# Kernel optimization log

Hardware: AMD Instinct MI355X
Metric: run time of the kernel (lower is better)

Reference implementation:

```python
import jax, jax.numpy as jnp
import numpy as np

P = 12           # AR order == number of rollout steps
N = 2048         # input_size (nodes)
B = 128          # batch
C = 1            # channels (only channel 0 used)


def setup_inputs() -> dict:
    key = jax.random.key(0)
    kx, kw = jax.random.split(key)
    x = jax.random.normal(kx, (B, N, C, P), dtype=jnp.float32)
    W = jax.random.normal(kw, (P, N, N), dtype=jnp.float32)
    return {"x": x, "W": W}


def reference(x, W):
    # x: [B, N, C, L]; take channel 0 and transpose -> [B, L(=p), N]
    xt = jnp.transpose(x[:, :, 0, :], (0, 2, 1))

    def step(xc, _):
        # einsum('ijk,bik->bij') followed by sum over i fuses to 'ijk,bik->bj'
        y = jnp.einsum('ijk,bik->bj', W, xc)              # [B, N]
        xc = jnp.concatenate([xc[:, 1:, :], y[:, None, :]], axis=1)  # shift window
        return xc, y

    _, ys = jax.lax.scan(step, xt, None, length=12)       # ys: [12, B, N]
    return jnp.transpose(ys, (1, 2, 0))                   # [B, N, 12]
```

## Files before the change

kernel.cpp:

```cpp
#include <hip/hip_runtime.h>
#include <hip/hip_bf16.h>
#include <stdint.h>


typedef _Float16 f16x8 __attribute__((ext_vector_type(8)));
typedef float    f32x4 __attribute__((ext_vector_type(4)));

#define B_ 128
#define N_ 2048
#define P_ 12
#define K_ (P_*N_)
#define KSPLIT 48
#define KCH (K_/KSPLIT)
#define NPHASE (KCH/64)

#define WPK_BYTES   ((size_t)P_*N_*N_*2)
#define H_SLOT_BYTES ((size_t)B_*N_*2)
#define H_BYTES     (23*H_SLOT_BYTES)
#define PART_BYTES  ((size_t)KSPLIT*B_*N_*4)
#define WS_NEEDED   (WPK_BYTES + H_BYTES + PART_BYTES)

__device__ __constant__ int E_TAB[11] = {7, 13, 18, 24, 29, 35, 40, 46, 51, 57, 62};

__device__ __forceinline__ int e_of_slot(int g) {
    return (g < 12) ? 0 : E_TAB[g - 12];
}
__device__ __forceinline__ float pow2f(int e) {
    return __uint_as_float((uint32_t)(127 + e) << 23);
}

union F16x8 { _Float16 h[8]; uint4 q; };
union F16x4 { _Float16 h[4]; uint2 q; };

__device__ __forceinline__ uint32_t h_off(int slot, int b, int k) {
    uint32_t t = (uint32_t)((b << 6) + ((k & 31) << 1)) ^ (uint32_t)((b & 7) << 4);
    return (uint32_t)slot * (uint32_t)H_SLOT_BYTES + (uint32_t)(k >> 5) * (B_ * 64) + t;
}

__global__ void prep_w(const float* __restrict__ W, char* __restrict__ Wp) {
    __shared__ float tile[64][68];
    int id = blockIdx.x;
    int i  = id >> 10;
    int rem = id & 1023;
    int jt = rem >> 5, kt = rem & 31;
    int j0 = jt * 64, k0 = kt * 64;
    int t = threadIdx.x;
    #pragma unroll
    for (int pass = 0; pass < 4; ++pass) {
        int jl = pass * 16 + (t >> 4);
        int kq = (t & 15) * 4;
        float4 v = *(const float4*)(W + ((size_t)i * N_ + (j0 + jl)) * N_ + k0 + kq);
        tile[jl][kq + 0] = v.x; tile[jl][kq + 1] = v.y;
        tile[jl][kq + 2] = v.z; tile[jl][kq + 3] = v.w;
    }
    __syncthreads();
    #pragma unroll
    for (int pass = 0; pass < 2; ++pass) {
        int itx = pass * 256 + t;
        int jl = itx & 63, kb = itx >> 6;
        F16x8 o;
        #pragma unroll
        for (int q = 0; q < 8; ++q) o.h[q] = (_Float16)tile[jl][kb * 8 + q];
        size_t kgblk = (size_t)i * 256 + (size_t)kt * 8 + kb;
        size_t off = (kgblk * N_ + (size_t)(j0 + jl)) * 16;
        *(uint4*)(Wp + off) = o.q;
    }
}

__global__ void prep_x(const float* __restrict__ x, char* __restrict__ H) {
    int tid = blockIdx.x * 256 + threadIdx.x;
    int b = tid >> 8;
    int n0 = (tid & 255) << 3;
    const float4* s4 = (const float4*)(x + ((size_t)b * N_ + n0) * P_);
    float4 tmp[24];
    #pragma unroll
    for (int i2 = 0; i2 < 24; ++i2) tmp[i2] = s4[i2];
    #pragma unroll
    for (int p = 0; p < 12; ++p) {
        F16x8 o;
        #pragma unroll
        for (int q = 0; q < 8; ++q) {
            int fi = q * 12 + p;
            float4 blk = tmp[fi >> 2];
            float f = ((fi & 3) == 0) ? blk.x : ((fi & 3) == 1) ? blk.y : ((fi & 3) == 2) ? blk.z : blk.w;
            o.h[q] = (_Float16)f;
        }
        *(uint4*)(H + h_off(p, b, n0)) = o.q;
    }
}

__global__ __launch_bounds__(256, 3) void gemm_step(
        const char* __restrict__ Wp, const char* __restrict__ H,
        float* __restrict__ partial, int t)
{
    __shared__ alignas(16) char ldsA[2][16384];
    const int tid  = threadIdx.x;
    const int lane = tid & 63;
    const int wv   = tid >> 6;
    const int wr   = wv >> 1;
    const int wc   = wv & 1;
    const int bid  = blockIdx.x;
    const int ks    = bid % KSPLIT;
    const int ntile = bid / KSPLIT;
    const int jbase = (ntile << 7) + (wc << 6) + (lane & 15);
    const int ko   = lane >> 4;
    const int kbase = ks * KCH;

    uint32_t aoff[4];
    #pragma unroll
    for (int mf = 0; mf < 4; ++mf) {
        int row = (wr << 6) + (mf << 4) + (lane & 15);
        aoff[mf] = (uint32_t)((row << 6) + (ko << 4)) ^ (uint32_t)((row & 7) << 4);
    }

    auto stage = [&](int buf, int ph) {
        int kg = kbase + (ph << 6);
        int slot = t + (kg >> 11);
        uint32_t srcb = (uint32_t)slot * (uint32_t)H_SLOT_BYTES
                      + (uint32_t)((kg & 2047) >> 5) * 8192u;
        #pragma unroll
        for (int j = 0; j < 4; ++j) {
            uint32_t o = (uint32_t)(j << 12) + (uint32_t)(wv << 10) + (uint32_t)(lane << 4);
            __builtin_amdgcn_global_load_lds(
                (const __attribute__((address_space(1))) void*)(H + srcb + o),
                (__attribute__((address_space(3))) void*)&ldsA[buf][(j << 12) + (wv << 10)], 16, 0, 0);
        }
    };
    auto loadB = [&](int ph, int ksub, f16x8* bh) {
        #pragma unroll
        for (int nf = 0; nf < 4; ++nf) {
            size_t kgblk = (size_t)(ks * 64 + ph * 8 + ksub * 4 + ko);
            size_t o = (kgblk * N_ + (size_t)(jbase + nf * 16)) * 16;
            bh[nf] = *(const f16x8*)(Wp + o);
        }
    };

    f32x4 acc[4][4];
    #pragma unroll
    for (int m = 0; m < 4; ++m)
        #pragma unroll
        for (int n = 0; n < 4; ++n) acc[m][n] = (f32x4){0.f, 0.f, 0.f, 0.f};

    f16x8 bhA[4], bhB[4];
    stage(0, 0);
    loadB(0, 0, bhA);
    __syncthreads();

    auto compute = [&](const char* lb, int ksub, const f16x8* bh) {
        #pragma unroll
        for (int m = 0; m < 4; ++m) {
            f16x8 ah = *(const f16x8*)(lb + (ksub << 13) + aoff[m]);
            #pragma unroll
            for (int n = 0; n < 4; ++n)
                acc[m][n] = __builtin_amdgcn_mfma_f32_16x16x32_f16(ah, bh[n], acc[m][n], 0, 0, 0);
        }
    };

    for (int ph = 0; ph < NPHASE; ++ph) {
        const char* lb = &ldsA[ph & 1][0];
        if (ph + 1 < NPHASE) stage((ph & 1) ^ 1, ph + 1);
        loadB(ph, 1, bhB);
        compute(lb, 0, bhA);
        if (ph + 1 < NPHASE) loadB(ph + 1, 0, bhA);
        compute(lb, 1, bhB);
        __syncthreads();
    }

    const int r0 = (lane >> 4) << 2;
    float* pb = partial + ((size_t)ks * B_ + (wr << 6) + r0) * N_ + jbase;
    #pragma unroll
    for (int m = 0; m < 4; ++m)
        #pragma unroll
        for (int n = 0; n < 4; ++n)
            #pragma unroll
            for (int r = 0; r < 4; ++r)
                pb[(size_t)(m * 16 + r) * N_ + n * 16] = acc[m][n][r];
}

__global__ void reduce_step(const float* __restrict__ partial, float* __restrict__ out,
                            char* __restrict__ H, int t)
{
    int tid = blockIdx.x * 256 + threadIdx.x;
    int b = tid >> 9;
    int n0 = (tid & 511) << 2;
    float s0 = 0.f, s1 = 0.f, s2 = 0.f, s3 = 0.f;
    #pragma unroll 4
    for (int ksI = 0; ksI < KSPLIT; ++ksI) {
        float sc = pow2f(e_of_slot(t + (ksI >> 2)));
        float4 a = *(const float4*)(partial + ((size_t)ksI * B_ + b) * N_ + n0);
        s0 += a.x * sc; s1 += a.y * sc; s2 += a.z * sc; s3 += a.w * sc;
    }
    float* ob = out + ((size_t)b * N_ + n0) * P_ + t;
    ob[0 * P_] = s0; ob[1 * P_] = s1; ob[2 * P_] = s2; ob[3 * P_] = s3;
    if (t < 11) {
        float ds = pow2f(-E_TAB[t]);
        F16x4 o;
        o.h[0] = (_Float16)(s0 * ds); o.h[1] = (_Float16)(s1 * ds);
        o.h[2] = (_Float16)(s2 * ds); o.h[3] = (_Float16)(s3 * ds);
        *(uint2*)(H + h_off(12 + t, b, n0)) = o.q;
    }
}

__global__ void naive_step(const float* __restrict__ x, const float* __restrict__ W,
                           float* __restrict__ out, int t)
{
    int tid = blockIdx.x * 256 + threadIdx.x;
    int b = tid >> 11;
    int j = tid & (N_ - 1);
    float acc = 0.f;
    for (int i = 0; i < 12; ++i) {
        int g = t + i;
        const float* src = (g < 12) ? (x   + (size_t)b * (N_ * 12) + g)
                                    : (out + (size_t)b * (N_ * 12) + (g - 12));
        const float* wr = W + ((size_t)i * N_ + j) * N_;
        for (int k = 0; k < N_; ++k)
            acc += wr[k] * src[(size_t)k * 12];
    }
    out[((size_t)b * N_ + j) * 12 + t] = acc;
}

extern "C" void kernel_launch(void* const* d_in, const int* in_sizes, int n_in,
                              void* d_out, int out_size, void* d_ws, size_t ws_size,
                              hipStream_t stream)
{
    const float* x = (const float*)d_in[0];
    const float* W = (const float*)d_in[1];
    float* out = (float*)d_out;

    if (ws_size < WS_NEEDED) {
        for (int t = 0; t < 12; ++t)
            naive_step<<<1024, 256, 0, stream>>>(x, W, out, t);
        return;
    }

    char* ws = (char*)d_ws;
    char* Wp = ws;
    char* H  = Wp + WPK_BYTES;
    float* partial = (float*)(H + H_BYTES);

    prep_w<<<12288, 256, 0, stream>>>(W, Wp);
    prep_x<<<128, 256, 0, stream>>>(x, H);
    for (int t = 0; t < 12; ++t) {
        gemm_step<<<768, 256, 0, stream>>>(Wp, H, partial, t);
        reduce_step<<<256, 256, 0, stream>>>(partial, out, H, t);
    }
}
```

Baseline: 499.0 us.

## Stage W tiles through LDS and read activations directly from global

W is repacked into per-N-tile, per-k-phase 16KB swizzled tiles, so each gemm block streams contiguous W tiles into LDS with global_load_lds. The activation matrix H is now read straight from global into registers, using a new layout that makes those loads coalesced. The goal is fully contiguous, LDS-staged transfers for the large W operand instead of strided direct register loads. In exchange, H reads are no longer shared through LDS across waves, and the larger register prefetch may raise register pressure.

New measurement: 508.4 us. Within noise of the previous version (+1.9%).

```diff
diff --git a/kernel.cpp b/kernel.cpp
--- a/kernel.cpp
+++ b/kernel.cpp
@@ -13,8 +13,10 @@
 #define KSPLIT 48
 #define KCH (K_/KSPLIT)
 #define NPHASE (KCH/64)
-
-#define WPK_BYTES   ((size_t)P_*N_*N_*2)
+#define NTILES 16
+#define NKP (K_/64)
+
+#define WPK_BYTES   ((size_t)NTILES*NKP*16384)
 #define H_SLOT_BYTES ((size_t)B_*N_*2)
 #define H_BYTES     (23*H_SLOT_BYTES)
 #define PART_BYTES  ((size_t)KSPLIT*B_*N_*4)
@@ -33,20 +35,25 @@
 union F16x4 { _Float16 h[4]; uint2 q; };
 
 __device__ __forceinline__ uint32_t h_off(int slot, int b, int k) {
-    uint32_t t = (uint32_t)((b << 6) + ((k & 31) << 1)) ^ (uint32_t)((b & 7) << 4);
-    return (uint32_t)slot * (uint32_t)H_SLOT_BYTES + (uint32_t)(k >> 5) * (B_ * 64) + t;
+    return (uint32_t)slot * (uint32_t)H_SLOT_BYTES
+         + (uint32_t)(k >> 5) * 8192u + (uint32_t)(((k >> 3) & 3) << 11)
+         + (uint32_t)(b << 4) + (uint32_t)((k & 7) << 1);
+}
+
+__device__ __forceinline__ size_t w_tile_base(int nt, int pk) {
+    return ((size_t)nt * NKP + (size_t)pk) * 16384;
 }
 
 __global__ void prep_w(const float* __restrict__ W, char* __restrict__ Wp) {
-    __shared__ float tile[64][68];
+    __shared__ float tile[128][68];
     int id = blockIdx.x;
-    int i  = id >> 10;
-    int rem = id & 1023;
-    int jt = rem >> 5, kt = rem & 31;
-    int j0 = jt * 64, k0 = kt * 64;
+    int nt = id / NKP, pk = id % NKP;
+    int i = pk >> 5;
+    int k0 = (pk & 31) << 6;
+    int j0 = nt << 7;
     int t = threadIdx.x;
     #pragma unroll
-    for (int pass = 0; pass < 4; ++pass) {
+    for (int pass = 0; pass < 8; ++pass) {
         int jl = pass * 16 + (t >> 4);
         int kq = (t & 15) * 4;
         float4 v = *(const float4*)(W + ((size_t)i * N_ + (j0 + jl)) * N_ + k0 + kq);
@@ -54,16 +61,15 @@
         tile[jl][kq + 2] = v.z; tile[jl][kq + 3] = v.w;
     }
     __syncthreads();
-    #pragma unroll
-    for (int pass = 0; pass < 2; ++pass) {
-        int itx = pass * 256 + t;
-        int jl = itx & 63, kb = itx >> 6;
+    int ksub = t >> 7, c = t & 127;
+    char* base = Wp + w_tile_base(nt, pk) + (ksub << 13);
+    #pragma unroll
+    for (int ko = 0; ko < 4; ++ko) {
         F16x8 o;
         #pragma unroll
-        for (int q = 0; q < 8; ++q) o.h[q] = (_Float16)tile[jl][kb * 8 + q];
-        size_t kgblk = (size_t)i * 256 + (size_t)kt * 8 + kb;
-        size_t off = (kgblk * N_ + (size_t)(j0 + jl)) * 16;
-        *(uint4*)(Wp + off) = o.q;
+        for (int q = 0; q < 8; ++q) o.h[q] = (_Float16)tile[c][ksub * 32 + ko * 8 + q];
+        uint32_t off = (uint32_t)((c << 6) + (ko << 4)) ^ (uint32_t)((c & 7) << 4);
+        *(uint4*)(base + off) = o.q;
     }
 }
 
@@ -91,9 +97,9 @@
 
 __global__ __launch_bounds__(256, 3) void gemm_step(
         const char* __restrict__ Wp, const char* __restrict__ H,
-        float* __restrict__ partial, int t)
-{
-    __shared__ alignas(16) char ldsA[2][16384];
+        float* __restrict__ partial, int st)
+{
+    __shared__ alignas(16) char ldsB[2][16384];
     const int tid  = threadIdx.x;
     const int lane = tid & 63;
     const int wv   = tid >> 6;
@@ -105,33 +111,36 @@
     const int jbase = (ntile << 7) + (wc << 6) + (lane & 15);
     const int ko   = lane >> 4;
     const int kbase = ks * KCH;
-
-    uint32_t aoff[4];
-    #pragma unroll
-    for (int mf = 0; mf < 4; ++mf) {
-        int row = (wr << 6) + (mf << 4) + (lane & 15);
-        aoff[mf] = (uint32_t)((row << 6) + (ko << 4)) ^ (uint32_t)((row & 7) << 4);
+    const int pk0  = kbase >> 6;
+
+    uint32_t boff[4];
+    #pragma unroll
+    for (int nf = 0; nf < 4; ++nf) {
+        int c = (wc << 6) + (nf << 4) + (lane & 15);
+        boff[nf] = (uint32_t)((c << 6) + (ko << 4)) ^ (uint32_t)((c & 7) << 4);
     }
 
     auto stage = [&](int buf, int ph) {
-        int kg = kbase + (ph << 6);
-        int slot = t + (kg >> 11);
-        uint32_t srcb = (uint32_t)slot * (uint32_t)H_SLOT_BYTES
-                      + (uint32_t)((kg & 2047) >> 5) * 8192u;
+        const char* src = Wp + w_tile_base(ntile, pk0 + ph);
         #pragma unroll
         for (int j = 0; j < 4; ++j) {
-            uint32_t o = (uint32_t)(j << 12) + (uint32_t)(wv << 10) + (uint32_t)(lane << 4);
+            uint32_t o = (uint32_t)(j << 12) + (uint32_t)(tid << 4);
             __builtin_amdgcn_global_load_lds(
-                (const __attribute__((address_space(1))) void*)(H + srcb + o),
-                (__attribute__((address_space(3))) void*)&ldsA[buf][(j << 12) + (wv << 10)], 16, 0, 0);
+                (const __attribute__((address_space(1))) void*)(src + o),
+                (__attribute__((address_space(3))) void*)&ldsB[buf][(j << 12) + (wv << 10)], 16, 0, 0);
         }
     };
-    auto loadB = [&](int ph, int ksub, f16x8* bh) {
-        #pragma unroll
-        for (int nf = 0; nf < 4; ++nf) {
-            size_t kgblk = (size_t)(ks * 64 + ph * 8 + ksub * 4 + ko);
-            size_t o = (kgblk * N_ + (size_t)(jbase + nf * 16)) * 16;
-            bh[nf] = *(const f16x8*)(Wp + o);
+    auto loadA = [&](int ph, f16x8 a[2][4]) {
+        #pragma unroll
+        for (int ksub = 0; ksub < 2; ++ksub) {
+            int kg = kbase + (ph << 6) + (ksub << 5);
+            const char* sb = H + (size_t)(st + (kg >> 11)) * H_SLOT_BYTES
+                           + (uint32_t)(((kg & 2047) >> 5) << 13) + (uint32_t)(ko << 11);
+            #pragma unroll
+            for (int m = 0; m < 4; ++m) {
+                int brow = (wr << 6) + (m << 4) + (lane & 15);
+                a[ksub][m] = *(const f16x8*)(sb + (brow << 4));
+            }
         }
     };
 
@@ -141,28 +150,33 @@
         #pragma unroll
         for (int n = 0; n < 4; ++n) acc[m][n] = (f32x4){0.f, 0.f, 0.f, 0.f};
 
-    f16x8 bhA[4], bhB[4];
+    f16x8 a[2][4];
+    loadA(0, a);
     stage(0, 0);
-    loadB(0, 0, bhA);
     __syncthreads();
 
-    auto compute = [&](const char* lb, int ksub, const f16x8* bh) {
-        #pragma unroll
-        for (int m = 0; m < 4; ++m) {
-            f16x8 ah = *(const f16x8*)(lb + (ksub << 13) + aoff[m]);
-            #pragma unroll
-            for (int n = 0; n < 4; ++n)
-                acc[m][n] = __builtin_amdgcn_mfma_f32_16x16x32_f16(ah, bh[n], acc[m][n], 0, 0, 0);
-        }
-    };
-
     for (int ph = 0; ph < NPHASE; ++ph) {
-        const char* lb = &ldsA[ph & 1][0];
         if (ph + 1 < NPHASE) stage((ph & 1) ^ 1, ph + 1);
-        loadB(ph, 1, bhB);
-        compute(lb, 0, bhA);
-        if (ph + 1 < NPHASE) loadB(ph + 1, 0, bhA);
-        compute(lb, 1, bhB);
+        const char* lb = &ldsB[ph & 1][0];
+        f16x8 bf[2][4];
+        #pragma unroll
+        for (int ksub = 0; ksub < 2; ++ksub)
+            #pragma unroll
+            for (int nf = 0; nf < 4; ++nf)
+                bf[ksub][nf] = *(const f16x8*)(lb + (ksub << 13) + boff[nf]);
+        f16x8 an[2][4];
+        if (ph + 1 < NPHASE) loadA(ph + 1, an);
+        #pragma unroll
+        for (int ksub = 0; ksub < 2; ++ksub)
+            #pragma unroll
+            for (int m = 0; m < 4; ++m)
+                #pragma unroll
+                for (int nf = 0; nf < 4; ++nf)
+                    acc[m][nf] = __builtin_amdgcn_mfma_f32_16x16x32_f16(a[ksub][m], bf[ksub][nf], acc[m][nf], 0, 0, 0);
+        #pragma unroll
+        for (int ksub = 0; ksub < 2; ++ksub)
+            #pragma unroll
+            for (int m = 0; m < 4; ++m) a[ksub][m] = an[ksub][m];
         __syncthreads();
     }
 
@@ -238,7 +252,7 @@
     char* H  = Wp + WPK_BYTES;
     float* partial = (float*)(H + H_BYTES);
 
-    prep_w<<<12288, 256, 0, stream>>>(W, Wp);
+    prep_w<<<6144, 256, 0, stream>>>(W, Wp);
     prep_x<<<128, 256, 0, stream>>>(x, H);
     for (int t = 0; t < 12; ++t) {
         gemm_step<<<768, 256, 0, stream>>>(Wp, H, partial, t);
```
